# Kernel tuning notes

Measured on AMD Instinct MI355X. Metric: run time of the kernel, lower is better.

Reference implementation:

```python
import math
import jax, jax.numpy as jnp
import numpy as np

NEG_INF = -1e9


def maximum_path(neg_cent, text_len, spec_len):
    """Monotonic alignment search (VITS). neg_cent: [B, Ty(spec), Tx(text)].
    Returns hard path [B, Ty, Tx] (float32, 0/1)."""
    B, Ty, Tx = neg_cent.shape
    xs = jnp.arange(Tx)

    # Forward DP over spec frames y; carry = best cumulative value per text pos x.
    def fwd_step(value, inp):
        y, score = inp  # score: [B, Tx]
        diag = jnp.pad(value[:, :-1], ((0, 0), (1, 0)), constant_values=NEG_INF)
        d = diag > value  # move-diagonally indicator for backtracking
        new = score + jnp.maximum(value, diag)
        new = jnp.where(y == 0, jnp.where(xs == 0, score, NEG_INF), new)
        return new, d

    init = jnp.full((B, Tx), NEG_INF, dtype=neg_cent.dtype)
    _, dirs = jax.lax.scan(fwd_step, init,
                           (jnp.arange(Ty), jnp.swapaxes(neg_cent, 0, 1)))
    # dirs: [Ty, B, Tx] bool; dirs[y] compares row y-1 values (as in cython MAS).

    # Backtrack from (spec_len-1, text_len-1) down to y=0.
    def bwd_step(index, inp):
        y, d_row = inp  # index: [B] int32, d_row: [B, Tx]
        active = y < spec_len  # [B]
        row = jnp.where(active[:, None],
                        jax.nn.one_hot(index, Tx, dtype=jnp.float32), 0.0)
        d_at = jnp.take_along_axis(d_row, index[:, None], axis=1)[:, 0]
        move = (index != 0) & ((index == y) | d_at)
        index = jnp.where(active & move, index - 1, index)
        return index, row

    init_idx = text_len - 1
    _, path = jax.lax.scan(bwd_step, init_idx, (jnp.arange(Ty), dirs),
                           reverse=True)
    return jnp.swapaxes(path, 0, 1)  # [B, Ty, Tx]


def setup_inputs() -> dict:
    key = jax.random.key(0)
    ks = jax.random.split(key, 6)
    B, C, Tx, Ty = 8, 192, 512, 2048
    z_p = jax.random.normal(ks[0], (B, C, Ty), dtype=jnp.float32)
    m_p = jax.random.normal(ks[1], (B, C, Tx), dtype=jnp.float32)
    logs_p = 0.1 * jax.random.normal(ks[2], (B, C, Tx), dtype=jnp.float32)
    logs_q = 0.1 * jax.random.normal(ks[3], (B, C, Ty), dtype=jnp.float32)
    text_len = jax.random.randint(ks[4], (B,), Tx * 3 // 4, Tx + 1)
    spec_len = jax.random.randint(ks[5], (B,), Ty * 3 // 4, Ty + 1)
    text_mask = (jnp.arange(Tx)[None, :] < text_len[:, None]).astype(jnp.float32)[:, None, :]
    spec_mask = (jnp.arange(Ty)[None, :] < spec_len[:, None]).astype(jnp.float32)[:, None, :]
    return {"z_p": z_p, "m_p": m_p, "logs_p": logs_p, "logs_q": logs_q,
            "text_mask": text_mask, "spec_mask": spec_mask}


def reference(z_p, m_p, logs_p, logs_q, text_mask, spec_mask):
    text_len = jnp.sum(text_mask, axis=(1, 2)).astype(jnp.int32)  # [B]
    spec_len = jnp.sum(spec_mask, axis=(1, 2)).astype(jnp.int32)  # [B]

    # ---- search_path: neg log-likelihood grid [B, T_spec, T_text] ----
    s_p_sq_r = jnp.exp(-2.0 * logs_p)  # [B, C, Tx]
    nc1 = jnp.sum(-0.5 * math.log(2 * math.pi) - logs_p, axis=1, keepdims=True)  # [B,1,Tx]
    nc2 = jnp.einsum('bct,bcx->btx', -0.5 * z_p * z_p, s_p_sq_r)
    nc3 = jnp.einsum('bct,bcx->btx', z_p, m_p * s_p_sq_r)
    nc4 = jnp.sum(-0.5 * m_p * m_p * s_p_sq_r, axis=1, keepdims=True)  # [B,1,Tx]
    neg_cent = nc1 + nc2 + nc3 + nc4  # [B, Ty, Tx]

    MAS_path = maximum_path(neg_cent, text_len, spec_len)  # [B, Ty, Tx]

    # ---- gather-combine text stats onto spec frames ----
    m_p_a = jnp.einsum('btx,bcx->bct', MAS_path, m_p)      # [B, C, Ty]
    logs_p_a = jnp.einsum('btx,bcx->bct', MAS_path, logs_p)

    # ---- KL divergence loss (VITS) ----
    kl = logs_p_a - logs_q - 0.5 \
        + 0.5 * jnp.square(z_p - m_p_a) * jnp.exp(-2.0 * logs_p_a)
    loss_kl = jnp.sum(kl * spec_mask) / jnp.sum(spec_mask)

    duration = jnp.sum(MAS_path, axis=1)[:, None, :]  # [B, 1, Tx]
    return MAS_path[:, None], m_p_a, logs_p_a, loss_kl, duration
```

## Files before the change

### kernel.cpp

```cpp
#include <hip/hip_runtime.h>
#include <cstdint>
#include <cstddef>

#define BB 8
#define CC 192
#define TXX 512
#define TYY 2048

#define NEG_INF (-1e9f)
#define HALF_LOG_2PI 0.9189385332046727f

#define O1 8388608
#define O2 11534336
#define O3 14680064
#define O4 14680065

#define WS_NEG   0
#define WS_S     33554432
#define WS_MSR   36700160
#define WS_BIAS  39845888
#define WS_DIRS  39862272
#define WS_IDX   40910848
#define WS_LENS  40976384
#define WS_PART  40976448

typedef float f32x4 __attribute__((ext_vector_type(4)));

#define PRE_NPREP 3072
#define PRE_NBIAS 16
#define PRE_NLEN  8
__global__ __launch_bounds__(256) void k_pre(const float* __restrict__ logs_p,
                                             const float* __restrict__ m_p,
                                             const float* __restrict__ tmask,
                                             const float* __restrict__ smask,
                                             float* __restrict__ s,
                                             float* __restrict__ msr,
                                             float* __restrict__ bias,
                                             int* __restrict__ lens) {
    int blk = blockIdx.x, tid = threadIdx.x;
    if (blk < PRE_NPREP) {
        int i = blk * 256 + tid;
        float lp = logs_p[i], m = m_p[i];
        float sv = expf(-2.0f * lp);
        s[i] = sv;
        msr[i] = m * sv;
    } else if (blk < PRE_NPREP + PRE_NBIAS) {
        int i = (blk - PRE_NPREP) * 256 + tid;
        int b = i >> 9, x = i & (TXX - 1);
        size_t base = (size_t)b * CC * TXX + x;
        const float* lpb = logs_p + base;
        const float* mb  = m_p + base;
        float acc = 0.f;
#pragma unroll 8
        for (int c = 0; c < CC; ++c) {
            float lp = lpb[(size_t)c * TXX];
            float m  = mb[(size_t)c * TXX];
            float msv = m * expf(-2.0f * lp);
            acc += -HALF_LOG_2PI - lp - 0.5f * m * msv;
        }
        bias[i] = acc;
    } else {
        __shared__ float red[256];
        int b = blk - (PRE_NPREP + PRE_NBIAS);
        float ts = 0.f;
        for (int i = tid; i < TXX; i += 256) ts += tmask[b * TXX + i];
        red[tid] = ts; __syncthreads();
        for (int s2 = 128; s2 > 0; s2 >>= 1) { if (tid < s2) red[tid] += red[tid + s2]; __syncthreads(); }
        if (tid == 0) lens[b] = (int)(red[0] + 0.5f);
        __syncthreads();
        float ss = 0.f;
        for (int i = tid; i < TYY; i += 256) ss += smask[b * TYY + i];
        red[tid] = ss; __syncthreads();
        for (int s2 = 128; s2 > 0; s2 >>= 1) { if (tid < s2) red[tid] += red[tid + s2]; __syncthreads(); }
        if (tid == 0) lens[8 + b] = (int)(red[0] + 0.5f);
    }
}

#define GZ_NZERO 512
__global__ __launch_bounds__(256) void k_gz(const float* __restrict__ z,
                                            const float* __restrict__ msr,
                                            const float* __restrict__ sarr,
                                            const float* __restrict__ bias,
                                            const int* __restrict__ lens,
                                            float* __restrict__ neg,
                                            float* __restrict__ out) {
    int id = blockIdx.x, tid = threadIdx.x;
    if (id < GZ_NZERO) {
        int64_t i = (int64_t)id * 256 + tid;
        const int64_t n4 = (int64_t)BB * TYY * TXX / 4;
        float4 z4 = make_float4(0.f, 0.f, 0.f, 0.f);
        float4* p4 = (float4*)out;
        for (int64_t k = i; k < n4; k += (int64_t)GZ_NZERO * 256) p4[k] = z4;
        if (i < BB * TXX) out[O4 + i] = 0.0f;
        return;
    }
    int gid = id - GZ_NZERO;
    int x0 = (gid & 7) * 64, t0 = ((gid >> 3) & 31) * 64, b = gid >> 8;
    if (x0 >= lens[b] || t0 >= lens[8 + b]) return;

    __shared__ float Zs[16][68], Ms[16][68], Ss[16][68];
    int tx = tid & 15, ty = tid >> 4;
    const float* zb = z    + (size_t)b * CC * TYY;
    const float* mb = msr  + (size_t)b * CC * TXX;
    const float* sb = sarr + (size_t)b * CC * TXX;
    int lr = tid >> 4, lc = (tid & 15) * 4;
    float acc[4][4] = {};
    float4 zv = *(const float4*)(zb + (size_t)lr * TYY + t0 + lc);
    float4 mv = *(const float4*)(mb + (size_t)lr * TXX + x0 + lc);
    float4 sv = *(const float4*)(sb + (size_t)lr * TXX + x0 + lc);
    for (int k0 = 0; k0 < CC; k0 += 16) {
        __syncthreads();
        *(float4*)&Zs[lr][lc] = zv;
        *(float4*)&Ms[lr][lc] = mv;
        *(float4*)&Ss[lr][lc] = sv;
        __syncthreads();
        if (k0 + 16 < CC) {
            zv = *(const float4*)(zb + (size_t)(k0 + 16 + lr) * TYY + t0 + lc);
            mv = *(const float4*)(mb + (size_t)(k0 + 16 + lr) * TXX + x0 + lc);
            sv = *(const float4*)(sb + (size_t)(k0 + 16 + lr) * TXX + x0 + lc);
        }
#pragma unroll
        for (int k = 0; k < 16; ++k) {
            float4 a4  = *(const float4*)&Zs[k][ty * 4];
            float4 bm4 = *(const float4*)&Ms[k][tx * 4];
            float4 bs4 = *(const float4*)&Ss[k][tx * 4];
            float av[4]  = {a4.x, a4.y, a4.z, a4.w};
            float bmv[4] = {bm4.x, bm4.y, bm4.z, bm4.w};
            float bsv[4] = {bs4.x, bs4.y, bs4.z, bs4.w};
#pragma unroll
            for (int i2 = 0; i2 < 4; ++i2) {
                float a2 = -0.5f * av[i2] * av[i2];
#pragma unroll
                for (int j = 0; j < 4; ++j)
                    acc[i2][j] += av[i2] * bmv[j] + a2 * bsv[j];
            }
        }
    }
    float4 b4 = *(const float4*)(bias + b * TXX + x0 + tx * 4);
    float bv[4] = {b4.x, b4.y, b4.z, b4.w};
#pragma unroll
    for (int i2 = 0; i2 < 4; ++i2) {
        int t = t0 + ty * 4 + i2;
        float4 o;
        o.x = acc[i2][0] + bv[0]; o.y = acc[i2][1] + bv[1];
        o.z = acc[i2][2] + bv[2]; o.w = acc[i2][3] + bv[3];
        *(float4*)(neg + ((size_t)b * TYY + t) * TXX + x0 + tx * 4) = o;
    }
}

#define GLOAD4(DST, PTR, OFF)                                             \
    asm volatile("global_load_dwordx4 %0, %1, off offset:" #OFF           \
                 : "=v"(DST) : "v"(PTR) : "memory")

#define GLOADD(DST, PTR)                                                  \
    asm volatile("global_load_dword %0, %1, off"                          \
                 : "=v"(DST) : "v"(PTR) : "memory")

#define WAIT_VM(N) do {                                                   \
    asm volatile("s_waitcnt vmcnt(" #N ")" ::: "memory");                 \
    __builtin_amdgcn_sched_barrier(0);                                    \
} while (0)

#define LOADG(DST, G) do {                                                \
    const char* p0_ = (const char*)nc4 + (size_t)(G) * 16384 + lane * 32; \
    const char* p2_ = p0_ + 4096;                                         \
    const char* p4_ = p0_ + 8192;                                         \
    const char* p6_ = p0_ + 12288;                                        \
    GLOAD4(DST[0],  p0_, 0);    GLOAD4(DST[1],  p0_, 16);                 \
    GLOAD4(DST[2],  p0_, 2048); GLOAD4(DST[3],  p0_, 2064);               \
    GLOAD4(DST[4],  p2_, 0);    GLOAD4(DST[5],  p2_, 16);                 \
    GLOAD4(DST[6],  p2_, 2048); GLOAD4(DST[7],  p2_, 2064);               \
    GLOAD4(DST[8],  p4_, 0);    GLOAD4(DST[9],  p4_, 16);                 \
    GLOAD4(DST[10], p4_, 2048); GLOAD4(DST[11], p4_, 2064);               \
    GLOAD4(DST[12], p6_, 0);    GLOAD4(DST[13], p6_, 16);                 \
    GLOAD4(DST[14], p6_, 2048); GLOAD4(DST[15], p6_, 2064);               \
} while (0)

#define DPROW(CUR, YB, R) do {                                                \
    int y_ = (YB) + (R);                                                      \
    float s0_ = CUR[2*(R)][0],   s1_ = CUR[2*(R)][1];                         \
    float s2_ = CUR[2*(R)][2],   s3_ = CUR[2*(R)][3];                         \
    float s4_ = CUR[2*(R)+1][0], s5_ = CUR[2*(R)+1][1];                       \
    float s6_ = CUR[2*(R)+1][2], s7_ = CUR[2*(R)+1][3];                       \
    unsigned d_ = 0;                                                          \
    if (y_ == 0) {                                                            \
        if (lane == 0) v[0] = s0_;             \
    } else {                                                                  \
        float pl_ = __int_as_float(__builtin_amdgcn_update_dpp(               \
            0, __float_as_int(v[7]), 0x138, 0xF, 0xF, false));                \
        if (lane == 0) pl_ = NEG_INF;                                         \
        float n0_ = s0_ + fmaxf(v[0], pl_);  if (pl_  > v[0]) d_ |= 1u;       \
        float n1_ = s1_ + fmaxf(v[1], v[0]); if (v[0] > v[1]) d_ |= 2u;       \
        float n2_ = s2_ + fmaxf(v[2], v[1]); if (v[1] > v[2]) d_ |= 4u;       \
        float n3_ = s3_ + fmaxf(v[3], v[2]); if (v[2] > v[3]) d_ |= 8u;       \
        float n4_ = s4_ + fmaxf(v[4], v[3]); if (v[3] > v[4]) d_ |= 16u;      \
        float n5_ = s5_ + fmaxf(v[5], v[4]); if (v[4] > v[5]) d_ |= 32u;      \
        float n6_ = s6_ + fmaxf(v[6], v[5]); if (v[5] > v[6]) d_ |= 64u;      \
        float n7_ = s7_ + fmaxf(v[7], v[6]); if (v[6] > v[7]) d_ |= 128u;     \
        v[0] = n0_; v[1] = n1_; v[2] = n2_; v[3] = n3_;                       \
        v[4] = n4_; v[5] = n5_; v[6] = n6_; v[7] = n7_;                       \
    }                                                                         \
    unsigned t_ = (unsigned)(y_ - 8 * lane);                                  \
    if (t_ < 8u) d_ |= 1u << t_;                 \
    acc |= d_ << (((R) & 3) * 8);                                             \
    if (((R) & 3) == 3) { db32[(y_ >> 2) * 64 + lane] = acc; acc = 0; }       \
} while (0)

#define FWD_ITER(G, CUR, NXT) do {                                \
    int g_ = (G);                                                 \
    if (g_ + 2 < ng) {                                            \
        LOADG(NXT, g_ + 2);                 \
        WAIT_VM(32);                                              \
    } else if (g_ + 1 < ng) {                                     \
        WAIT_VM(16);                                              \
    } else {                                                      \
        WAIT_VM(0);                                               \
    }                                                             \
    int yb_ = 8 * g_;                                             \
    DPROW(CUR, yb_, 0); DPROW(CUR, yb_, 1);                       \
    DPROW(CUR, yb_, 2); DPROW(CUR, yb_, 3);                       \
    DPROW(CUR, yb_, 4); DPROW(CUR, yb_, 5);                       \
    DPROW(CUR, yb_, 6); DPROW(CUR, yb_, 7);                       \
} while (0)

__global__ __launch_bounds__(64, 1) void k_fwd(const float* __restrict__ neg,
                                               const int* __restrict__ lens,
                                               uint32_t* __restrict__ dirs) {
    int b = blockIdx.x, lane = threadIdx.x;
    const float* nc4 = neg + (size_t)b * TYY * TXX;
    uint32_t* db32 = dirs + (size_t)b * (TYY / 4) * 64;
    int slen = lens[8 + b];
    int ng = (slen + 7) >> 3;

    float v[8];
#pragma unroll
    for (int j = 0; j < 8; ++j) v[j] = NEG_INF;
    unsigned acc = 0;

    f32x4 bufA[16], bufB[16], bufC[16];
    LOADG(bufA, 0);
    LOADG(bufB, 1);

    for (int p = 0; p < ng; p += 3) {
        FWD_ITER(p, bufA, bufC);
        if (p + 1 < ng) FWD_ITER(p + 1, bufB, bufA);
        if (p + 2 < ng) FWD_ITER(p + 2, bufC, bufB);
    }
}

#define RAWLD(NR, WB, QROW) do {                                          \
    const uint32_t* p_ = db32 + (QROW) + 4 * (WB);                        \
    GLOADD(NR[0],  (p_ + 0));  GLOADD(NR[1],  (p_ + 1));                  \
    GLOADD(NR[2],  (p_ + 2));  GLOADD(NR[3],  (p_ + 3));                  \
    GLOADD(NR[4],  (p_ + 4));  GLOADD(NR[5],  (p_ + 5));                  \
    GLOADD(NR[6],  (p_ + 6));  GLOADD(NR[7],  (p_ + 7));                  \
    GLOADD(NR[8],  (p_ + 8));  GLOADD(NR[9],  (p_ + 9));                  \
    GLOADD(NR[10], (p_ + 10)); GLOADD(NR[11], (p_ + 11));                 \
} while (0)

#define PACKW(W0, W1, W2, NR, BOFF) do {                                  \
    W0 = ((NR[0]>>(BOFF))&0xffu)        | (((NR[1]>>(BOFF))&0xffu)<<8) |  \
         (((NR[2]>>(BOFF))&0xffu)<<16)  | (((NR[3]>>(BOFF))&0xffu)<<24);  \
    W1 = ((NR[4]>>(BOFF))&0xffu)        | (((NR[5]>>(BOFF))&0xffu)<<8) |  \
         (((NR[6]>>(BOFF))&0xffu)<<16)  | (((NR[7]>>(BOFF))&0xffu)<<24);  \
    W2 = ((NR[8]>>(BOFF))&0xffu)        | (((NR[9]>>(BOFF))&0xffu)<<8) |  \
         (((NR[10]>>(BOFF))&0xffu)<<16) | (((NR[11]>>(BOFF))&0xffu)<<24); \
} while (0)

__global__ __launch_bounds__(64, 1) void k_bwd(const int* __restrict__ lens,
                                               const uint32_t* __restrict__ dirs,
                                               int* __restrict__ idx_map,
                                               float* __restrict__ out) {
    int b = blockIdx.x, lane = threadIdx.x;
    const uint32_t* db32 = dirs + (size_t)b * (TYY / 4) * 64;
    int tlen = lens[b], slen = lens[8 + b];

    int idx = tlen - 1;
    int y0 = slen - 1;
    int wb;
    uint32_t W0 = 0, W1 = 0, W2 = 0;
    {
        int yy = y0 - lane; if (yy < 0) yy = 0;
        int qrow = (yy >> 2) * 64, boff = (yy & 3) * 8;
        int t = (idx >> 5) - 1; if (t < 0) t = 0; if (t > 13) t = 13;
        wb = t;
        uint32_t R[12];
        if (lane < 32) {
            RAWLD(R, wb, qrow);
            asm volatile("s_waitcnt vmcnt(0)" ::: "memory");
            __builtin_amdgcn_sched_barrier(0);
            PACKW(W0, W1, W2, R, boff);
        }
    }
    while (y0 >= 0) {
        int w0 = (idx >> 5) - 1; if (w0 < 0) w0 = 0; if (w0 > 14) w0 = 14;
        int s = w0 - wb; if (s < 0) s = 0; if (s > 1) s = 1;
        uint32_t lo = s ? W1 : W0;
        uint32_t hi = s ? W2 : W1;
        int base = (wb + s) << 5;
        uint32_t N[12];
        int idxm = idx - 32; if (idxm < 0) idxm = 0;
        int wbn = (idxm >> 5) - 1; if (wbn < 0) wbn = 0; if (wbn > 13) wbn = 13;
        int yn = y0 - 32 - lane; if (yn < 0) yn = 0;
        int qn = (yn >> 2) * 64, bn = (yn & 3) * 8;
        if (lane < 32) RAWLD(N, wbn, qn);
        __builtin_amdgcn_sched_barrier(0);
        int nsteps = (y0 + 1 < 32) ? y0 + 1 : 32;
        int cap = 0;
#pragma unroll
        for (int j = 0; j < 32; ++j) {
            if (lane == j) cap = idx;
            uint32_t l = (uint32_t)__builtin_amdgcn_readlane((int)lo, j);
            uint32_t h = (uint32_t)__builtin_amdgcn_readlane((int)hi, j);
            int bp = idx - base;
            uint32_t word = (bp & 32) ? h : l;
            idx -= (int)((word >> (bp & 31)) & 1u);
        }
        __builtin_amdgcn_sched_barrier(0);
        asm volatile("s_waitcnt vmcnt(0)" ::: "memory");
        __builtin_amdgcn_sched_barrier(0);
        PACKW(W0, W1, W2, N, bn);
        wb = wbn;
        if (lane < nsteps) {
            int y = y0 - lane;
            idx_map[b * TYY + y] = cap;
            out[((size_t)(b * TYY + y)) * TXX + cap] = 1.0f;
            atomicAdd(&out[O4 + b * TXX + cap], 1.0f);
        }
        y0 -= 32;
    }
}

__global__ __launch_bounds__(256) void k_gather(const float* __restrict__ z_p,
                                                const float* __restrict__ m_p,
                                                const float* __restrict__ logs_p,
                                                const float* __restrict__ logs_q,
                                                const int* __restrict__ lens,
                                                const int* __restrict__ idx_map,
                                                float* __restrict__ out,
                                                float* __restrict__ partials) {
    const int S = BB * CC * TYY / 4;
    int base = blockIdx.x * 256 + threadIdx.x;
    float klsum = 0.f;
#pragma unroll
    for (int r = 0; r < 4; ++r) {
        int i = base + r * S;
        int t = i & (TYY - 1);
        int bc = i >> 11;
        int b = bc / CC;
        float ma = 0.f, la = 0.f;
        if (t < lens[8 + b]) {
            int x = idx_map[b * TYY + t];
            size_t off = (size_t)bc * TXX + x;
            ma = m_p[off];
            la = logs_p[off];
            float zv = z_p[i], lq = logs_q[i];
            float dz = zv - ma;
            klsum += la - lq - 0.5f + 0.5f * dz * dz * expf(-2.0f * la);
        }
        out[O1 + i] = ma;
        out[O2 + i] = la;
    }
    for (int o = 32; o > 0; o >>= 1) klsum += __shfl_down(klsum, o);
    __shared__ float red[4];
    if ((threadIdx.x & 63) == 0) red[threadIdx.x >> 6] = klsum;
    __syncthreads();
    if (threadIdx.x == 0) partials[blockIdx.x] = red[0] + red[1] + red[2] + red[3];
}

__global__ void k_final(const float* __restrict__ partials, const int* __restrict__ lens,
                        float* __restrict__ out) {
    float s = 0.f;
    for (int i = threadIdx.x; i < 3072; i += 256) s += partials[i];
    for (int o = 32; o > 0; o >>= 1) s += __shfl_down(s, o);
    __shared__ float red[4];
    if ((threadIdx.x & 63) == 0) red[threadIdx.x >> 6] = s;
    __syncthreads();
    if (threadIdx.x == 0) {
        float tot = 0.f;
        for (int b = 0; b < 8; ++b) tot += (float)lens[8 + b];
        out[O3] = (red[0] + red[1] + red[2] + red[3]) / tot;
    }
}

extern "C" void kernel_launch(void* const* d_in, const int* in_sizes, int n_in,
                              void* d_out, int out_size, void* d_ws, size_t ws_size,
                              hipStream_t stream) {
    const float* z_p    = (const float*)d_in[0];
    const float* m_p    = (const float*)d_in[1];
    const float* logs_p = (const float*)d_in[2];
    const float* logs_q = (const float*)d_in[3];
    const float* tmask  = (const float*)d_in[4];
    const float* smask  = (const float*)d_in[5];
    float* out = (float*)d_out;
    char* ws = (char*)d_ws;

    float*    neg      = (float*)(ws + WS_NEG);
    float*    sarr     = (float*)(ws + WS_S);
    float*    msr      = (float*)(ws + WS_MSR);
    float*    bias     = (float*)(ws + WS_BIAS);
    uint32_t* dirs     = (uint32_t*)(ws + WS_DIRS);
    int*      idx_map  = (int*)(ws + WS_IDX);
    int*      lens     = (int*)(ws + WS_LENS);
    float*    partials = (float*)(ws + WS_PART);

    hipLaunchKernelGGL(k_pre,    dim3(PRE_NPREP + PRE_NBIAS + PRE_NLEN),
                       dim3(256), 0, stream,
                       logs_p, m_p, tmask, smask, sarr, msr, bias, lens);
    hipLaunchKernelGGL(k_gz,     dim3(GZ_NZERO + 2048), dim3(256), 0, stream,
                       z_p, msr, sarr, bias, lens, neg, out);
    hipLaunchKernelGGL(k_fwd,    dim3(8),        dim3(64),  0, stream, neg, lens, dirs);
    hipLaunchKernelGGL(k_bwd,    dim3(8),        dim3(64),  0, stream, lens, dirs, idx_map, out);
    hipLaunchKernelGGL(k_gather, dim3(3072),     dim3(256), 0, stream,
                       z_p, m_p, logs_p, logs_q, lens, idx_map, out, partials);
    hipLaunchKernelGGL(k_final,  dim3(1),        dim3(256), 0, stream, partials, lens, out);
}
```

Measured before the change: 488.4 us.

## Split forward MAS DP across two waves with wavefront pipelining via LDS flags

The forward DP kernel now uses two waves per batch, each owning half of the text axis (4 columns per lane instead of 8). Wave A hands its boundary column value to wave B through a small shared-memory ring, and the two waves step through row groups in a skewed pipeline coordinated by acquire/release flag polling. The aim is to halve the serial per-row work on the critical path of this latency-bound kernel. In exchange it adds flag spin-waits, sleeps and extra DPP shuffles to pack direction bits across lane pairs, and wave A may run at most a bounded number of groups ahead of wave B.

```diff
diff --git a/kernel.cpp b/kernel.cpp
--- a/kernel.cpp
+++ b/kernel.cpp
@@ -162,82 +162,118 @@
 } while (0)
 
 #define LOADG(DST, G) do {                                                \
-    const char* p0_ = (const char*)nc4 + (size_t)(G) * 16384 + lane * 32; \
+    const char* p0_ = ncb + (size_t)(G) * 16384;                          \
     const char* p2_ = p0_ + 4096;                                         \
     const char* p4_ = p0_ + 8192;                                         \
     const char* p6_ = p0_ + 12288;                                        \
-    GLOAD4(DST[0],  p0_, 0);    GLOAD4(DST[1],  p0_, 16);                 \
-    GLOAD4(DST[2],  p0_, 2048); GLOAD4(DST[3],  p0_, 2064);               \
-    GLOAD4(DST[4],  p2_, 0);    GLOAD4(DST[5],  p2_, 16);                 \
-    GLOAD4(DST[6],  p2_, 2048); GLOAD4(DST[7],  p2_, 2064);               \
-    GLOAD4(DST[8],  p4_, 0);    GLOAD4(DST[9],  p4_, 16);                 \
-    GLOAD4(DST[10], p4_, 2048); GLOAD4(DST[11], p4_, 2064);               \
-    GLOAD4(DST[12], p6_, 0);    GLOAD4(DST[13], p6_, 16);                 \
-    GLOAD4(DST[14], p6_, 2048); GLOAD4(DST[15], p6_, 2064);               \
-} while (0)
-
-#define DPROW(CUR, YB, R) do {                                                \
-    int y_ = (YB) + (R);                                                      \
-    float s0_ = CUR[2*(R)][0],   s1_ = CUR[2*(R)][1];                         \
-    float s2_ = CUR[2*(R)][2],   s3_ = CUR[2*(R)][3];                         \
-    float s4_ = CUR[2*(R)+1][0], s5_ = CUR[2*(R)+1][1];                       \
-    float s6_ = CUR[2*(R)+1][2], s7_ = CUR[2*(R)+1][3];                       \
+    GLOAD4(DST[0], p0_, 0); GLOAD4(DST[1], p0_, 2048);                    \
+    GLOAD4(DST[2], p2_, 0); GLOAD4(DST[3], p2_, 2048);                    \
+    GLOAD4(DST[4], p4_, 0); GLOAD4(DST[5], p4_, 2048);                    \
+    GLOAD4(DST[6], p6_, 0); GLOAD4(DST[7], p6_, 2048);                    \
+} while (0)
+
+#define POLL_GE(FLAG, VAL) do {                                           \
+    while (__hip_atomic_load(&(FLAG), __ATOMIC_ACQUIRE,                   \
+                             __HIP_MEMORY_SCOPE_WORKGROUP) < (VAL))       \
+        __builtin_amdgcn_s_sleep(1);                                      \
+    __builtin_amdgcn_sched_barrier(0);                                    \
+} while (0)
+
+#define SET_FLAG(FLAG, VAL) do {                                          \
+    asm volatile("s_waitcnt lgkmcnt(0)" ::: "memory");                    \
+    __builtin_amdgcn_sched_barrier(0);                                    \
+    if (lane == 0)                                                        \
+        __hip_atomic_store(&(FLAG), (VAL), __ATOMIC_RELEASE,              \
+                           __HIP_MEMORY_SCOPE_WORKGROUP);                 \
+} while (0)
+
+#define DPR4(BUF, R, YB) do {                                                 \
+    f32x4 q_ = BUF[R];                                                        \
     unsigned d_ = 0;                                                          \
-    if (y_ == 0) {                                                            \
-        if (lane == 0) v[0] = s0_;             \
+    float pl_ = __int_as_float(__builtin_amdgcn_update_dpp(                   \
+        ninf_i, __float_as_int(v[3]), 0x138, 0xF, 0xF, false));               \
+    if (!isA && lane == 0) pl_ = bnv[R];                                      \
+    float n0_ = q_[0] + fmaxf(v[0], pl_);  if (pl_  > v[0]) d_ |= 1u;         \
+    float n1_ = q_[1] + fmaxf(v[1], v[0]); if (v[0] > v[1]) d_ |= 2u;         \
+    float n2_ = q_[2] + fmaxf(v[2], v[1]); if (v[1] > v[2]) d_ |= 4u;         \
+    float n3_ = q_[3] + fmaxf(v[3], v[2]); if (v[2] > v[3]) d_ |= 8u;         \
+    v[0] = n0_; v[1] = n1_; v[2] = n2_; v[3] = n3_;                           \
+    unsigned t_ = (unsigned)((YB) + (R) - xb4);                               \
+    if (t_ < 4u) d_ |= 1u << t_;                               \
+    unsigned dl_ = (unsigned)__builtin_amdgcn_update_dpp(                     \
+        0, (int)d_, 0x138, 0xF, 0xF, false);                                  \
+    acc |= ((d_ << 4) | dl_) << (((R) & 3) * 8);                              \
+    if (isA && lane == 63) bnd[((YB) + (R)) & 63] = v[3];                     \
+} while (0)
+
+#define DPR0(Q0) do {                                                         \
+    if (isA && lane == 0) v[0] = Q0[0];                                       \
+    unsigned d_ = (isA && lane == 0) ? 1u : 0u;                               \
+    unsigned dl_ = (unsigned)__builtin_amdgcn_update_dpp(                     \
+        0, (int)d_, 0x138, 0xF, 0xF, false);                                  \
+    acc |= (d_ << 4) | dl_;                                                   \
+    if (isA && lane == 63) bnd[0] = v[3];                                     \
+} while (0)
+
+#define FWD_ITER(G, CUR, NXT) do {                                            \
+    int g_ = (G);                                                             \
+    if (g_ + 2 < ng) LOADG(NXT, g_ + 2);               \
+    if (isA) { POLL_GE(flagB, g_ - 6); }                                      \
+    else     { POLL_GE(flagA, g_ + 1); }                                      \
+    float bnv[8];                                                             \
+    {   int bb_ = 8 * g_ - 1;                                                 \
+        _Pragma("unroll")                                                     \
+        for (int k_ = 0; k_ < 8; ++k_) bnv[k_] = bnd[(bb_ + k_) & 63]; }      \
+    __builtin_amdgcn_sched_barrier(0);                                        \
+    if (g_ + 2 < ng) { if (g_ < 2) { WAIT_VM(16); } else { WAIT_VM(20); } }   \
+    else if (g_ + 1 < ng) { WAIT_VM(12); }                                    \
+    else { WAIT_VM(4); }                                                      \
+    int yb_ = 8 * g_;                                                         \
+    uint32_t* dp_ = db32 + ((unsigned)g_ << 7) + woff + (lane >> 1);          \
+    if (yb_ == 0) {                                                           \
+        DPR0(CUR[0]);                                                         \
+        DPR4(CUR, 1, yb_); DPR4(CUR, 2, yb_); DPR4(CUR, 3, yb_);              \
     } else {                                                                  \
-        float pl_ = __int_as_float(__builtin_amdgcn_update_dpp(               \
-            0, __float_as_int(v[7]), 0x138, 0xF, 0xF, false));                \
-        if (lane == 0) pl_ = NEG_INF;                                         \
-        float n0_ = s0_ + fmaxf(v[0], pl_);  if (pl_  > v[0]) d_ |= 1u;       \
-        float n1_ = s1_ + fmaxf(v[1], v[0]); if (v[0] > v[1]) d_ |= 2u;       \
-        float n2_ = s2_ + fmaxf(v[2], v[1]); if (v[1] > v[2]) d_ |= 4u;       \
-        float n3_ = s3_ + fmaxf(v[3], v[2]); if (v[2] > v[3]) d_ |= 8u;       \
-        float n4_ = s4_ + fmaxf(v[4], v[3]); if (v[3] > v[4]) d_ |= 16u;      \
-        float n5_ = s5_ + fmaxf(v[5], v[4]); if (v[4] > v[5]) d_ |= 32u;      \
-        float n6_ = s6_ + fmaxf(v[6], v[5]); if (v[5] > v[6]) d_ |= 64u;      \
-        float n7_ = s7_ + fmaxf(v[7], v[6]); if (v[6] > v[7]) d_ |= 128u;     \
-        v[0] = n0_; v[1] = n1_; v[2] = n2_; v[3] = n3_;                       \
-        v[4] = n4_; v[5] = n5_; v[6] = n6_; v[7] = n7_;                       \
+        DPR4(CUR, 0, yb_); DPR4(CUR, 1, yb_);                                 \
+        DPR4(CUR, 2, yb_); DPR4(CUR, 3, yb_);                                 \
     }                                                                         \
-    unsigned t_ = (unsigned)(y_ - 8 * lane);                                  \
-    if (t_ < 8u) d_ |= 1u << t_;                 \
-    acc |= d_ << (((R) & 3) * 8);                                             \
-    if (((R) & 3) == 3) { db32[(y_ >> 2) * 64 + lane] = acc; acc = 0; }       \
-} while (0)
-
-#define FWD_ITER(G, CUR, NXT) do {                                \
-    int g_ = (G);                                                 \
-    if (g_ + 2 < ng) {                                            \
-        LOADG(NXT, g_ + 2);                 \
-        WAIT_VM(32);                                              \
-    } else if (g_ + 1 < ng) {                                     \
-        WAIT_VM(16);                                              \
-    } else {                                                      \
-        WAIT_VM(0);                                               \
-    }                                                             \
-    int yb_ = 8 * g_;                                             \
-    DPROW(CUR, yb_, 0); DPROW(CUR, yb_, 1);                       \
-    DPROW(CUR, yb_, 2); DPROW(CUR, yb_, 3);                       \
-    DPROW(CUR, yb_, 4); DPROW(CUR, yb_, 5);                       \
-    DPROW(CUR, yb_, 6); DPROW(CUR, yb_, 7);                       \
-} while (0)
-
-__global__ __launch_bounds__(64, 1) void k_fwd(const float* __restrict__ neg,
-                                               const int* __restrict__ lens,
-                                               uint32_t* __restrict__ dirs) {
-    int b = blockIdx.x, lane = threadIdx.x;
-    const float* nc4 = neg + (size_t)b * TYY * TXX;
+    if (lane & 1) dp_[0] = acc;                                               \
+    acc = 0;                                                                  \
+    DPR4(CUR, 4, yb_); DPR4(CUR, 5, yb_);                                     \
+    DPR4(CUR, 6, yb_); DPR4(CUR, 7, yb_);                                     \
+    if (lane & 1) dp_[64] = acc;                                              \
+    acc = 0;                                                                  \
+    if (isA) { SET_FLAG(flagA, g_ + 1); }                                     \
+    else     { SET_FLAG(flagB, g_ + 1); }                                     \
+} while (0)
+
+__global__ __launch_bounds__(128, 1) void k_fwd(const float* __restrict__ neg,
+                                                const int* __restrict__ lens,
+                                                uint32_t* __restrict__ dirs) {
+    __shared__ float bnd[64];
+    __shared__ int flagA, flagB;
+    int b = blockIdx.x, tid = threadIdx.x;
+    int wave = tid >> 6, lane = tid & 63;
+    bool isA = (wave == 0);
+    if (tid == 0) { flagA = 0; flagB = 0; }
+    __syncthreads();
+
+    int xhalf = isA ? 0 : 1024;
+    int xb4 = (isA ? 0 : 256) + 4 * lane;
+    int woff = isA ? 0 : 32;
+    const char* ncb = (const char*)(neg + (size_t)b * TYY * TXX)
+                      + xhalf + lane * 16;
     uint32_t* db32 = dirs + (size_t)b * (TYY / 4) * 64;
     int slen = lens[8 + b];
     int ng = (slen + 7) >> 3;
-
-    float v[8];
-#pragma unroll
-    for (int j = 0; j < 8; ++j) v[j] = NEG_INF;
+    int ninf_i = __float_as_int(NEG_INF);
+
+    float v[4];
+#pragma unroll
+    for (int j = 0; j < 4; ++j) v[j] = NEG_INF;
     unsigned acc = 0;
 
-    f32x4 bufA[16], bufB[16], bufC[16];
+    f32x4 bufA[8], bufB[8], bufC[8];
     LOADG(bufA, 0);
     LOADG(bufB, 1);
 
@@ -409,7 +445,7 @@
                        logs_p, m_p, tmask, smask, sarr, msr, bias, lens);
     hipLaunchKernelGGL(k_gz,     dim3(GZ_NZERO + 2048), dim3(256), 0, stream,
                        z_p, msr, sarr, bias, lens, neg, out);
-    hipLaunchKernelGGL(k_fwd,    dim3(8),        dim3(64),  0, stream, neg, lens, dirs);
+    hipLaunchKernelGGL(k_fwd,    dim3(8),        dim3(128), 0, stream, neg, lens, dirs);
     hipLaunchKernelGGL(k_bwd,    dim3(8),        dim3(64),  0, stream, lens, dirs, idx_map, out);
     hipLaunchKernelGGL(k_gather, dim3(3072),     dim3(256), 0, stream,
                        z_p, m_p, logs_p, logs_q, lens, idx_map, out, partials);
```

Measured after the change: 548.1 us. 1.12x slower.
